# Kernel optimization log

Hardware: AMD Instinct MI355X
Metric: run time of the kernel (lower is better)

The kernel has to match this reference:

```python
import jax, jax.numpy as jnp
import numpy as np

B, N, CIN, FOUT = 4, 512, 64, 64
EPS = 1e-5
NEG_SLOPE = 0.2


def setup_inputs() -> dict:
    key = jax.random.key(0)
    ks = jax.random.split(key, 10)
    s = lambda k, shape: (jax.random.normal(k, shape, dtype=jnp.float32) * 0.05)
    return {
        "x": jax.random.normal(ks[0], (B, N, CIN), dtype=jnp.float32),
        "adj": jax.random.uniform(ks[1], (N, N), dtype=jnp.float32),
        "W_w": s(ks[2], (FOUT, CIN)), "W_b": s(ks[3], (FOUT,)),
        "U_w": s(ks[4], (FOUT, FOUT)), "U_b": s(ks[5], (FOUT,)),
        "V_w": s(ks[6], (FOUT, FOUT)), "V_b": s(ks[7], (FOUT,)),
        "att_w": s(ks[8], (1, 2 * FOUT)), "att_b": s(ks[9], (1,)),
        "ln_g": jnp.ones((FOUT,), jnp.float32),
        "ln_b": jnp.zeros((FOUT,), jnp.float32),
    }


def reference(x, adj, W_w, W_b, U_w, U_b, V_w, V_b, att_w, att_b, ln_g, ln_b):
    # h = W(x): (B, N, F)
    h = x @ W_w.T + W_b
    Fd = h.shape[-1]
    # attention(cat[h_i, h_j]) == (h_i @ a_i) + (h_j @ a_j) + b  -> avoid (B,N,N,2F)
    a_i, a_j = att_w[0, :Fd], att_w[0, Fd:]
    logits = (h @ a_i)[:, :, None] + (h @ a_j)[:, None, :] + att_b[0]  # (B,N,N)
    logits = jnp.where(logits > 0, logits, NEG_SLOPE * logits)  # LeakyReLU(0.2)
    attn = jax.nn.softmax(logits, axis=-1)  # softmax over j; dropout is identity in eval
    # gate = sigmoid(U(h_i) + V(h_j)); U/V applied once per node then broadcast
    Uh = h @ U_w.T + U_b  # (B,N,F)
    Vh = h @ V_w.T + V_b  # (B,N,F)
    gate = jax.nn.sigmoid(Uh[:, :, None, :] + Vh[:, None, :, :])  # (B,N,N,F)
    node_features = gate * attn[..., None] * h[:, None, :, :]  # (B,N,N,F)
    # aggr[b,i,f] = sum_{j,k} nf[b,i,j,f] * adj[j,k]
    aggr = jnp.einsum('bijf,jk->bif', node_features, adj)
    # LayerNorm over last dim
    mu = jnp.mean(aggr, axis=-1, keepdims=True)
    var = jnp.var(aggr, axis=-1, keepdims=True)
    out = (aggr - mu) / jnp.sqrt(var + EPS) * ln_g + ln_b
    return out
```

## Files before the change

kernel.cpp:

```cpp
#include <hip/hip_runtime.h>

#define NB 4
#define NN 512
#define NF 64
#define NEG_SLOPE 0.2f
#define LN_EPS 1e-5f

__device__ __forceinline__ float wave_sum(float v){
  #pragma unroll
  for (int d = 32; d; d >>= 1) v += __shfl_xor(v, d, 64);
  return v;
}
__device__ __forceinline__ float wave_max(float v){
  #pragma unroll
  for (int d = 32; d; d >>= 1) v = fmaxf(v, __shfl_xor(v, d, 64));
  return v;
}


extern "C" __global__ __launch_bounds__(64)
void k_setup(const float* __restrict__ x, const float* __restrict__ adj,
             const float* __restrict__ Ww, const float* __restrict__ Wb,
             const float* __restrict__ Uw, const float* __restrict__ Ub,
             const float* __restrict__ Vw, const float* __restrict__ Vb,
             const float* __restrict__ attw,
             float* __restrict__ ws)
{
  float* r   = ws;
  float* evh = ws + NN;
  float* eU  = evh + NB*NN*NF*2;
  float* li  = eU + NB*NN*NF;
  float* lj  = li + NB*NN;

  const int blk  = blockIdx.x;
  const int lane = threadIdx.x;

  if (blk >= NB*NN) {
    int j = blk - NB*NN;
    const float2* a2 = (const float2*)(adj + j*NN);
    float s = 0.f;
    #pragma unroll
    for (int t = 0; t < 4; t++){
      float2 a = a2[lane + 64*t];
      s += a.x + a.y;
    }
    s = wave_sum(s);
    if (lane == 0) r[j] = s;
    return;
  }

  const int row = blk;
  __shared__ float sx[NF];
  __shared__ float sh[NF];

  sx[lane] = x[row*NF + lane];
  __syncthreads();

  float hv = Wb[lane];
  {
    const float4* w4 = (const float4*)(Ww + lane*NF);
    #pragma unroll
    for (int t = 0; t < 16; t++){
      float4 w = w4[t];
      hv = fmaf(sx[4*t+0], w.x, hv);
      hv = fmaf(sx[4*t+1], w.y, hv);
      hv = fmaf(sx[4*t+2], w.z, hv);
      hv = fmaf(sx[4*t+3], w.w, hv);
    }
  }
  sh[lane] = hv;
  __syncthreads();

  float uh = Ub[lane];
  float vh = Vb[lane];
  {
    const float4* u4 = (const float4*)(Uw + lane*NF);
    const float4* v4 = (const float4*)(Vw + lane*NF);
    #pragma unroll
    for (int t = 0; t < 16; t++){
      float4 uu = u4[t]; float4 vv = v4[t];
      float h0 = sh[4*t+0], h1 = sh[4*t+1], h2 = sh[4*t+2], h3 = sh[4*t+3];
      uh = fmaf(h0, uu.x, uh); vh = fmaf(h0, vv.x, vh);
      uh = fmaf(h1, uu.y, uh); vh = fmaf(h1, vv.y, vh);
      uh = fmaf(h2, uu.z, uh); vh = fmaf(h2, vv.z, vh);
      uh = fmaf(h3, uu.w, uh); vh = fmaf(h3, vv.w, vh);
    }
  }

  float ev = __expf(-vh);
  float eu = __expf(-uh);
  ((float2*)evh)[row*NF + lane] = make_float2(ev, hv);
  eU[row*NF + lane] = eu;

  float pi = wave_sum(hv * attw[lane]);
  float pj = wave_sum(hv * attw[NF + lane]);
  if (lane == 0){ li[row] = pi; lj[row] = pj; }
}

extern "C" __global__ __launch_bounds__(256)
void k_main(const float* __restrict__ attb_p,
            const float* __restrict__ lng,
            const float* __restrict__ lnb,
            const float* __restrict__ ws,
            float* __restrict__ out)
{
  const float* r   = ws;
  const float* evh = ws + NN;
  const float* eU  = evh + NB*NN*NF*2;
  const float* li  = eU + NB*NN*NF;
  const float* lj  = li + NB*NN;

  __shared__ float s_c[NN][4];
  __shared__ float s_part[4][4][NF];

  const int tid  = threadIdx.x;
  const int w    = tid >> 6;
  const int lane = tid & 63;
  const int b    = blockIdx.x >> 7;
  const int i0   = (blockIdx.x & 127) * 4;
  const int i    = i0 + w;

  const float attb = attb_p[0];
  const float li_s = li[b*NN + i];

  float lv[8];
  float m = -1e30f;
  #pragma unroll
  for (int t = 0; t < 8; t++){
    int j = lane + 64*t;
    float l = li_s + lj[b*NN + j] + attb;
    l = (l > 0.f) ? l : NEG_SLOPE*l;
    lv[t] = l;
    m = fmaxf(m, l);
  }
  m = wave_max(m);
  float S = 0.f;
  #pragma unroll
  for (int t = 0; t < 8; t++){ lv[t] = __expf(lv[t] - m); S += lv[t]; }
  S = wave_sum(S);
  float inv = __builtin_amdgcn_rcpf(S);
  #pragma unroll
  for (int t = 0; t < 8; t++){
    int j = lane + 64*t;
    s_c[j][w] = lv[t]*inv*r[j];
  }

  const float eu0 = eU[(b*NN + i0 + 0)*NF + lane];
  const float eu1 = eU[(b*NN + i0 + 1)*NF + lane];
  const float eu2 = eU[(b*NN + i0 + 2)*NF + lane];
  const float eu3 = eU[(b*NN + i0 + 3)*NF + lane];

  __syncthreads();

  const float2* evh2 = (const float2*)evh + (size_t)(b*NN)*NF;
  float a0 = 0.f, a1 = 0.f, a2 = 0.f, a3 = 0.f;
  const int j0 = w*128;
  #pragma unroll 8
  for (int jj = 0; jj < 128; jj++){
    int j = j0 + jj;
    float2 eh = evh2[j*NF + lane];
    float4 c4 = *(const float4*)&s_c[j][0];
    float q0 = fmaf(eu0, eh.x, 1.0f);
    float q1 = fmaf(eu1, eh.x, 1.0f);
    float q2 = fmaf(eu2, eh.x, 1.0f);
    float q3 = fmaf(eu3, eh.x, 1.0f);
    a0 = fmaf(c4.x, eh.y * __builtin_amdgcn_rcpf(q0), a0);
    a1 = fmaf(c4.y, eh.y * __builtin_amdgcn_rcpf(q1), a1);
    a2 = fmaf(c4.z, eh.y * __builtin_amdgcn_rcpf(q2), a2);
    a3 = fmaf(c4.w, eh.y * __builtin_amdgcn_rcpf(q3), a3);
  }

  s_part[w][0][lane] = a0;
  s_part[w][1][lane] = a1;
  s_part[w][2][lane] = a2;
  s_part[w][3][lane] = a3;
  __syncthreads();

  float acc = s_part[0][w][lane] + s_part[1][w][lane]
            + s_part[2][w][lane] + s_part[3][w][lane];

  float s1 = wave_sum(acc);
  float s2 = wave_sum(acc*acc);
  float mu  = s1 * (1.f/NF);
  float var = s2 * (1.f/NF) - mu*mu;
  float rs  = __builtin_amdgcn_rsqf(var + LN_EPS);
  float o = (acc - mu)*rs*lng[lane] + lnb[lane];
  out[(b*NN + i)*NF + lane] = o;
}

extern "C" void kernel_launch(void* const* d_in, const int* in_sizes, int n_in,
                              void* d_out, int out_size, void* d_ws, size_t ws_size,
                              hipStream_t stream)
{
  const float* x    = (const float*)d_in[0];
  const float* adj  = (const float*)d_in[1];
  const float* Ww   = (const float*)d_in[2];
  const float* Wb   = (const float*)d_in[3];
  const float* Uw   = (const float*)d_in[4];
  const float* Ub   = (const float*)d_in[5];
  const float* Vw   = (const float*)d_in[6];
  const float* Vb   = (const float*)d_in[7];
  const float* attw = (const float*)d_in[8];
  const float* attb = (const float*)d_in[9];
  const float* lng  = (const float*)d_in[10];
  const float* lnb  = (const float*)d_in[11];
  float* ws = (float*)d_ws;
  float* outp = (float*)d_out;

  hipLaunchKernelGGL(k_setup, dim3(NB*NN + NN), dim3(64), 0, stream,
                     x, adj, Ww, Wb, Uw, Ub, Vw, Vb, attw, ws);
  hipLaunchKernelGGL(k_main, dim3(NB*NN/4), dim3(256), 0, stream,
                     attb, lng, lnb, ws, outp);
}
```

Before: 103.7 us.

## Stage projection weights in LDS and process four rows per setup block

The setup kernel now runs 512 blocks of 256 threads instead of 2560 single-wave blocks. Each block loads W, U and V once into padded shared memory and computes four node rows, one per wave. The adjacency row-sum work is folded into the same blocks, one adj row per block. This cuts repeated global and L2 reads of the weight matrices and the block count, at the cost of about 50KB of LDS per block, which limits occupancy.

```diff
diff --git a/kernel.cpp b/kernel.cpp
--- a/kernel.cpp
+++ b/kernel.cpp
@@ -5,6 +5,7 @@
 #define NF 64
 #define NEG_SLOPE 0.2f
 #define LN_EPS 1e-5f
+#define WP 66
 
 __device__ __forceinline__ float wave_sum(float v){
   #pragma unroll
@@ -18,7 +19,7 @@
 }
 
 
-extern "C" __global__ __launch_bounds__(64)
+extern "C" __global__ __launch_bounds__(256, 2)
 void k_setup(const float* __restrict__ x, const float* __restrict__ adj,
              const float* __restrict__ Ww, const float* __restrict__ Wb,
              const float* __restrict__ Uw, const float* __restrict__ Ub,
@@ -32,58 +33,62 @@
   float* li  = eU + NB*NN*NF;
   float* lj  = li + NB*NN;
 
-  const int blk  = blockIdx.x;
-  const int lane = threadIdx.x;
-
-  if (blk >= NB*NN) {
-    int j = blk - NB*NN;
-    const float2* a2 = (const float2*)(adj + j*NN);
-    float s = 0.f;
+  __shared__ float s_w[3*64*WP];
+  __shared__ float s_x[4][NF];
+  __shared__ float s_h[4][NF];
+  __shared__ float s_red[4];
+
+  const int tid  = threadIdx.x;
+  const int w    = tid >> 6;
+  const int lane = tid & 63;
+  const int g    = blockIdx.x;
+  const int row  = g*4 + w;
+
+  {
+    const float4* srcs[3] = { (const float4*)Ww, (const float4*)Uw, (const float4*)Vw };
     #pragma unroll
-    for (int t = 0; t < 4; t++){
-      float2 a = a2[lane + 64*t];
-      s += a.x + a.y;
+    for (int m = 0; m < 3; m++){
+      const float4* src = srcs[m];
+      #pragma unroll
+      for (int k = 0; k < 4; k++){
+        int idx4 = tid + k*256;
+        float4 v = src[idx4];
+        int e = idx4 * 4;
+        int f = e >> 6, c = e & 63;
+        float* dst = &s_w[m*64*WP + f*WP + c];
+        dst[0] = v.x; dst[1] = v.y; dst[2] = v.z; dst[3] = v.w;
+      }
     }
-    s = wave_sum(s);
-    if (lane == 0) r[j] = s;
-    return;
-  }
-
-  const int row = blk;
-  __shared__ float sx[NF];
-  __shared__ float sh[NF];
-
-  sx[lane] = x[row*NF + lane];
+  }
+  s_x[w][lane] = x[row*NF + lane];
   __syncthreads();
 
   float hv = Wb[lane];
   {
-    const float4* w4 = (const float4*)(Ww + lane*NF);
+    const float* wr = &s_w[0*64*WP + lane*WP];
     #pragma unroll
-    for (int t = 0; t < 16; t++){
-      float4 w = w4[t];
-      hv = fmaf(sx[4*t+0], w.x, hv);
-      hv = fmaf(sx[4*t+1], w.y, hv);
-      hv = fmaf(sx[4*t+2], w.z, hv);
-      hv = fmaf(sx[4*t+3], w.w, hv);
+    for (int c = 0; c < NF; c += 2){
+      float2 xb = *(const float2*)&s_x[w][c];
+      float2 wv = *(const float2*)&wr[c];
+      hv = fmaf(xb.x, wv.x, hv);
+      hv = fmaf(xb.y, wv.y, hv);
     }
   }
-  sh[lane] = hv;
+  s_h[w][lane] = hv;
   __syncthreads();
 
   float uh = Ub[lane];
   float vh = Vb[lane];
   {
-    const float4* u4 = (const float4*)(Uw + lane*NF);
-    const float4* v4 = (const float4*)(Vw + lane*NF);
+    const float* ur = &s_w[1*64*WP + lane*WP];
+    const float* vr = &s_w[2*64*WP + lane*WP];
     #pragma unroll
-    for (int t = 0; t < 16; t++){
-      float4 uu = u4[t]; float4 vv = v4[t];
-      float h0 = sh[4*t+0], h1 = sh[4*t+1], h2 = sh[4*t+2], h3 = sh[4*t+3];
-      uh = fmaf(h0, uu.x, uh); vh = fmaf(h0, vv.x, vh);
-      uh = fmaf(h1, uu.y, uh); vh = fmaf(h1, vv.y, vh);
-      uh = fmaf(h2, uu.z, uh); vh = fmaf(h2, vv.z, vh);
-      uh = fmaf(h3, uu.w, uh); vh = fmaf(h3, vv.w, vh);
+    for (int c = 0; c < NF; c += 2){
+      float2 hb = *(const float2*)&s_h[w][c];
+      float2 uv = *(const float2*)&ur[c];
+      float2 vv = *(const float2*)&vr[c];
+      uh = fmaf(hb.x, uv.x, uh); uh = fmaf(hb.y, uv.y, uh);
+      vh = fmaf(hb.x, vv.x, vh); vh = fmaf(hb.y, vv.y, vh);
     }
   }
 
@@ -95,6 +100,15 @@
   float pi = wave_sum(hv * attw[lane]);
   float pj = wave_sum(hv * attw[NF + lane]);
   if (lane == 0){ li[row] = pi; lj[row] = pj; }
+
+  {
+    const float2* a2 = (const float2*)(adj + g*NN);
+    float2 a = a2[tid];
+    float s = wave_sum(a.x + a.y);
+    if (lane == 0) s_red[w] = s;
+    __syncthreads();
+    if (tid == 0) r[g] = s_red[0] + s_red[1] + s_red[2] + s_red[3];
+  }
 }
 
 extern "C" __global__ __launch_bounds__(256)
@@ -207,7 +221,7 @@
   float* ws = (float*)d_ws;
   float* outp = (float*)d_out;
 
-  hipLaunchKernelGGL(k_setup, dim3(NB*NN + NN), dim3(64), 0, stream,
+  hipLaunchKernelGGL(k_setup, dim3(NN), dim3(256), 0, stream,
                      x, adj, Ww, Wb, Uw, Ub, Vw, Vb, attw, ws);
   hipLaunchKernelGGL(k_main, dim3(NB*NN/4), dim3(256), 0, stream,
                      attb, lng, lnb, ws, outp);
```

New measurement: 98.44 us. -5.1%, faster.
